# Kernel optimization log

Measured on AMD Instinct MI355X. Metric: run time of the kernel, lower is better.

Reference implementation:

```python
import jax, jax.numpy as jnp
import numpy as np

N_NODES = 100000
N_EDGES = 1600000
D_IN = 128
D_HID = 128
D_OUT = 64


def setup_inputs() -> dict:
    key = jax.random.key(0)
    ks = jax.random.split(key, 8)
    x = jax.random.normal(ks[0], (N_NODES, D_IN), dtype=jnp.float32)
    edge_index = jax.random.randint(ks[1], (2, N_EDGES), 0, N_NODES, dtype=jnp.int64)
    s1 = 1.0 / np.sqrt(D_IN)
    s2 = 1.0 / np.sqrt(D_HID)
    W1_l = jax.random.normal(ks[2], (D_IN, D_HID), dtype=jnp.float32) * s1
    W1_r = jax.random.normal(ks[3], (D_IN, D_HID), dtype=jnp.float32) * s1
    b1 = jnp.zeros((D_HID,), dtype=jnp.float32)
    W2_l = jax.random.normal(ks[4], (D_HID, D_OUT), dtype=jnp.float32) * s2
    W2_r = jax.random.normal(ks[5], (D_HID, D_OUT), dtype=jnp.float32) * s2
    b2 = jnp.zeros((D_OUT,), dtype=jnp.float32)
    return {"x": x, "edge_index": edge_index, "W1_l": W1_l, "b1": b1,
            "W1_r": W1_r, "W2_l": W2_l, "b2": b2, "W2_r": W2_r}


def _sage_conv(x, src, dst, Wl, bl, Wr, num_nodes):
    # PyG SAGEConv (aggr='mean', root_weight=True):
    #   out = lin_l(mean_{j in N(i)} x_j) + lin_r(x_i)
    agg = jax.ops.segment_sum(x[src], dst, num_segments=num_nodes)        # [N, d]
    deg = jax.ops.segment_sum(jnp.ones((src.shape[0],), dtype=x.dtype), dst,
                              num_segments=num_nodes)                      # [N]
    mean = agg / jnp.maximum(deg, 1.0)[:, None]
    return mean @ Wl + bl + x @ Wr


def reference(x, edge_index, W1_l, b1, W1_r, W2_l, b2, W2_r):
    src, dst = edge_index[0], edge_index[1]
    n = x.shape[0]
    h = jax.nn.relu(_sage_conv(x, src, dst, W1_l, b1, W1_r, n))
    # dropout is identity in eval mode
    out = _sage_conv(h, src, dst, W2_l, b2, W2_r, n)
    return jax.nn.log_softmax(out, axis=1)
```

## Files before the change

kernel.cpp:

```cpp
#include <hip/hip_runtime.h>
#include <math.h>

#define NN 100000
#define NE 1600000
#define SBN 512
#define NSB ((NN + SBN - 1) / SBN)
#define SBCAP 10240
#define EPB 8192
#define NBA ((NE + EPB - 1) / EPB)

typedef __attribute__((ext_vector_type(8))) short bf16x8;
typedef __attribute__((ext_vector_type(8))) unsigned short ush8;
typedef __attribute__((ext_vector_type(4))) float f32x4;

static __device__ __forceinline__ float b2f(unsigned short u) {
    return __uint_as_float(((unsigned int)u) << 16);
}
static __device__ __forceinline__ unsigned short f2bf(float f) {
    unsigned int u = __float_as_uint(f);
    u += 0x7fffu + ((u >> 16) & 1u);
    return (unsigned short)(u >> 16);
}

__global__ __launch_bounds__(256)
void k_cvt_x(const float* __restrict__ in, unsigned short* __restrict__ outb, long total8) {
    long i = (long)blockIdx.x * 256 + threadIdx.x;
    long stride = (long)gridDim.x * 256;
    for (; i < total8; i += stride) {
        const float4* p = (const float4*)(in + i * 8);
        float4 a = p[0], b = p[1];
        ush8 r;
        r[0] = f2bf(a.x); r[1] = f2bf(a.y); r[2] = f2bf(a.z); r[3] = f2bf(a.w);
        r[4] = f2bf(b.x); r[5] = f2bf(b.y); r[6] = f2bf(b.z); r[7] = f2bf(b.w);
        *(ush8*)(outb + i * 8) = r;
    }
}

__global__ __launch_bounds__(256)
void k_cvt_w(const float* __restrict__ W, unsigned short* __restrict__ Wt, int N) {
    int id = blockIdx.x * 256 + threadIdx.x;
    if (id < N * 128) {
        int n = id >> 7, k = id & 127;
        Wt[id] = f2bf(W[k * N + n]);
    }
}

__global__ __launch_bounds__(1024)
void k_binA(const int* __restrict__ src, const int* __restrict__ dst,
            int* __restrict__ gcnt, int* __restrict__ pairs) {
    __shared__ int lsort[EPB];
    __shared__ int lhist[256];
    __shared__ int lofs[256];
    __shared__ int lpos[NSB];
    __shared__ int gbase[NSB];
    const int tid = threadIdx.x;
    const int base = blockIdx.x * EPB;
    const int cnt = min(EPB, NE - base);

    int v[8], bn[8];
    #pragma unroll
    for (int k = 0; k < 8; ++k) {
        int i = k * 1024 + tid;
        if (i < cnt) {
            int d = dst[base + i], s = src[base + i];
            v[k] = (s << 9) | (d & 511);
            bn[k] = d >> 9;
        } else bn[k] = -1;
    }
    if (tid < 256) lhist[tid] = 0;
    __syncthreads();
    #pragma unroll
    for (int k = 0; k < 8; ++k) if (bn[k] >= 0) atomicAdd(&lhist[bn[k]], 1);
    __syncthreads();
    if (tid < 256) lofs[tid] = lhist[tid];
    __syncthreads();
    for (int d = 1; d < 256; d <<= 1) {
        int u = (tid < 256 && tid >= d) ? lofs[tid - d] : 0;
        __syncthreads();
        if (tid < 256) lofs[tid] += u;
        __syncthreads();
    }
    if (tid < 256) lofs[tid] -= lhist[tid];
    __syncthreads();
    if (tid < NSB) {
        lpos[tid] = lofs[tid];
        gbase[tid] = atomicAdd(&gcnt[tid], lhist[tid]);
    }
    __syncthreads();
    #pragma unroll
    for (int k = 0; k < 8; ++k) if (bn[k] >= 0) {
        int slot = atomicAdd(&lpos[bn[k]], 1);
        lsort[slot] = v[k];
    }
    __syncthreads();
    for (int i = tid; i < cnt; i += 1024) {
        int lo = 0, hi = NSB - 1;
        while (lo < hi) { int mid = (lo + hi + 1) >> 1; if (lofs[mid] <= i) lo = mid; else hi = mid - 1; }
        int off = gbase[lo] + (i - lofs[lo]);
        if (off < SBCAP)
            __builtin_nontemporal_store(lsort[i], &pairs[(size_t)lo * SBCAP + off]);
    }
}

__global__ __launch_bounds__(1024)
void k_sortB(const int* __restrict__ gcnt, int* __restrict__ pairs,
             int* __restrict__ offs, int* __restrict__ deg) {
    __shared__ int lstage[SBCAP];
    __shared__ int lhist[SBN], lscan[SBN], lpos[SBN];
    const int sb = blockIdx.x, tid = threadIdx.x;
    const int cnt = min(gcnt[sb], SBCAP);
    int* __restrict__ region = pairs + (size_t)sb * SBCAP;

    for (int i = tid; i < cnt; i += 1024) lstage[i] = region[i];
    if (tid < SBN) lhist[tid] = 0;
    __syncthreads();
    for (int i = tid; i < cnt; i += 1024) atomicAdd(&lhist[lstage[i] & 511], 1);
    __syncthreads();
    if (tid < SBN) lscan[tid] = lhist[tid];
    __syncthreads();
    for (int d = 1; d < SBN; d <<= 1) {
        int u = (tid < SBN && tid >= d) ? lscan[tid - d] : 0;
        __syncthreads();
        if (tid < SBN) lscan[tid] += u;
        __syncthreads();
    }
    if (tid < SBN) {
        int ex = lscan[tid] - lhist[tid];
        lpos[tid] = ex;
        int node = sb * SBN + tid;
        if (node < NN) { offs[node] = sb * SBCAP + ex; deg[node] = lhist[tid]; }
    }
    __syncthreads();
    for (int i = tid; i < cnt; i += 1024) {
        int val = lstage[i];
        int slot = atomicAdd(&lpos[val & 511], 1);
        region[slot] = val >> 9;
    }
}

__global__ __launch_bounds__(256)
void k_aggregate_bf(const unsigned short* __restrict__ feat, const int* __restrict__ csr,
                    const int* __restrict__ offs, const int* __restrict__ deg,
                    unsigned short* __restrict__ outmean) {
    const int wid = threadIdx.x >> 6, lane = threadIdx.x & 63;
    const int q = lane >> 4, l4 = lane & 15;
    const int node = blockIdx.x * 4 + wid;
    if (node >= NN) return;
    int off = __builtin_amdgcn_readfirstlane(offs[node]);
    int dg  = __builtin_amdgcn_readfirstlane(deg[node]);
    const ush8* __restrict__ f8 = (const ush8*)feat;
    float acc[8];
    #pragma unroll
    for (int i = 0; i < 8; ++i) acc[i] = 0.f;
    int j = 0;
    for (; j + 8 <= dg; j += 8) {
        int e0 = csr[off + j + q];
        int e1 = csr[off + j + 4 + q];
        ush8 v0 = f8[(size_t)e0 * 16 + l4];
        ush8 v1 = f8[(size_t)e1 * 16 + l4];
        #pragma unroll
        for (int i = 0; i < 8; ++i) acc[i] += b2f(v0[i]) + b2f(v1[i]);
    }
    for (; j + 4 <= dg; j += 4) {
        int e0 = csr[off + j + q];
        ush8 v0 = f8[(size_t)e0 * 16 + l4];
        #pragma unroll
        for (int i = 0; i < 8; ++i) acc[i] += b2f(v0[i]);
    }
    int rem = dg - j;
    if (q < rem) {
        int e0 = csr[off + j + q];
        ush8 v0 = f8[(size_t)e0 * 16 + l4];
        #pragma unroll
        for (int i = 0; i < 8; ++i) acc[i] += b2f(v0[i]);
    }
    #pragma unroll
    for (int i = 0; i < 8; ++i) {
        acc[i] += __shfl_xor(acc[i], 16);
        acc[i] += __shfl_xor(acc[i], 32);
    }
    if (q == 0) {
        float inv = 1.0f / (float)(dg > 0 ? dg : 1);
        ush8 r;
        #pragma unroll
        for (int i = 0; i < 8; ++i) r[i] = f2bf(acc[i] * inv);
        ((ush8*)outmean)[(size_t)node * 16 + l4] = r;
    }
}

template <int BN, bool RELU, bool OUTBF, bool LSM>
__global__ __launch_bounds__(256)
void k_gemm_mfma(const unsigned short* __restrict__ Am, const unsigned short* __restrict__ Ax,
                 const unsigned short* __restrict__ Wtl, const unsigned short* __restrict__ Wtr,
                 const float* __restrict__ bias, void* __restrict__ outp) {
    constexpr int BM = 128;
    constexpr int WAVES_N = BN / 64;
    constexpr int WAVES_M = 4 / WAVES_N;
    constexpr int MR = BM / (WAVES_M * 16);
    constexpr int NR = 4;
    __shared__ __align__(16) short As[BM * 40];
    __shared__ __align__(16) short Ws[BN * 40];

    const int tid = threadIdx.x;
    const int wave = tid >> 6, lane = tid & 63;
    const int l15 = lane & 15, kg = lane >> 4;
    const int wc = wave % WAVES_N, wr = wave / WAVES_N;
    const int rowbase = wr * MR * 16;
    const int colbase = wc * 64;
    const int row0 = blockIdx.x * BM;

    f32x4 acc[MR][NR];
    #pragma unroll
    for (int mr = 0; mr < MR; ++mr)
        #pragma unroll
        for (int nr = 0; nr < NR; ++nr) acc[mr][nr] = (f32x4){0.f, 0.f, 0.f, 0.f};

    for (int s = 0; s < 2; ++s) {
        const unsigned short* __restrict__ A  = s ? Ax : Am;
        const unsigned short* __restrict__ Wt = s ? Wtr : Wtl;
        for (int kc = 0; kc < 128; kc += 32) {
            __syncthreads();
            #pragma unroll
            for (int i = 0; i < (BM * 4) / 256; ++i) {
                int c = tid + 256 * i; int r = c >> 2, g = c & 3;
                ush8 v = {0, 0, 0, 0, 0, 0, 0, 0};
                int grow = row0 + r;
                if (grow < NN) v = *(const ush8*)&A[(size_t)grow * 128 + kc + g * 8];
                *(ush8*)&As[r * 40 + g * 8] = v;
            }
            #pragma unroll
            for (int i = 0; i < (BN * 4) / 256; ++i) {
                int c = tid + 256 * i; int n = c >> 2, g = c & 3;
                *(ush8*)&Ws[n * 40 + g * 8] = *(const ush8*)&Wt[n * 128 + kc + g * 8];
            }
            __syncthreads();
            bf16x8 af[MR], bfr[NR];
            #pragma unroll
            for (int mr = 0; mr < MR; ++mr)
                af[mr] = *(const bf16x8*)&As[(rowbase + mr * 16 + l15) * 40 + kg * 8];
            #pragma unroll
            for (int nr = 0; nr < NR; ++nr)
                bfr[nr] = *(const bf16x8*)&Ws[(colbase + nr * 16 + l15) * 40 + kg * 8];
            #pragma unroll
            for (int mr = 0; mr < MR; ++mr)
                #pragma unroll
                for (int nr = 0; nr < NR; ++nr)
                    acc[mr][nr] = __builtin_amdgcn_mfma_f32_16x16x32_bf16(
                        af[mr], bfr[nr], acc[mr][nr], 0, 0, 0);
        }
    }
    const int r4 = kg * 4;
    if (LSM) {
        #pragma unroll
        for (int mr = 0; mr < MR; ++mr) {
            #pragma unroll
            for (int j = 0; j < 4; ++j) {
                int row = row0 + rowbase + mr * 16 + r4 + j;
                float v[NR];
                float m = -1e30f;
                #pragma unroll
                for (int nr = 0; nr < NR; ++nr) {
                    v[nr] = acc[mr][nr][j] + bias[nr * 16 + l15];
                    m = fmaxf(m, v[nr]);
                }
                #pragma unroll
                for (int d = 8; d >= 1; d >>= 1) m = fmaxf(m, __shfl_xor(m, d));
                float ssum = 0.f;
                #pragma unroll
                for (int nr = 0; nr < NR; ++nr) ssum += __expf(v[nr] - m);
                #pragma unroll
                for (int d = 8; d >= 1; d >>= 1) ssum += __shfl_xor(ssum, d);
                float lse = m + logf(ssum);
                if (row < NN) {
                    #pragma unroll
                    for (int nr = 0; nr < NR; ++nr)
                        ((float*)outp)[(size_t)row * 64 + nr * 16 + l15] = v[nr] - lse;
                }
            }
        }
    } else {
        #pragma unroll
        for (int mr = 0; mr < MR; ++mr) {
            #pragma unroll
            for (int nr = 0; nr < NR; ++nr) {
                int col = colbase + nr * 16 + l15;
                float bv = bias[col];
                #pragma unroll
                for (int j = 0; j < 4; ++j) {
                    int row = row0 + rowbase + mr * 16 + r4 + j;
                    if (row < NN) {
                        float v = acc[mr][nr][j] + bv;
                        if (RELU) v = fmaxf(v, 0.f);
                        if (OUTBF) ((unsigned short*)outp)[(size_t)row * BN + col] = f2bf(v);
                        else       ((float*)outp)[(size_t)row * BN + col] = v;
                    }
                }
            }
        }
    }
}

extern "C" void kernel_launch(void* const* d_in, const int* in_sizes, int n_in,
                              void* d_out, int out_size, void* d_ws, size_t ws_size,
                              hipStream_t stream) {
    const float* x   = (const float*)d_in[0];
    const int* edges = (const int*)d_in[1];
    const float* W1l = (const float*)d_in[2];
    const float* b1  = (const float*)d_in[3];
    const float* W1r = (const float*)d_in[4];
    const float* W2l = (const float*)d_in[5];
    const float* b2  = (const float*)d_in[6];
    const float* W2r = (const float*)d_in[7];
    float* out = (float*)d_out;

    const int* src = edges;
    const int* dst = edges + NE;

    char* ws = (char*)d_ws;
    size_t o = 0;
    auto alloc = [&](size_t bytes) -> void* {
        void* p = ws + o;
        o = (o + bytes + 255) & ~(size_t)255;
        return p;
    };
    int* gcnt  = (int*)alloc((size_t)NSB * 4);
    int* pairs = (int*)alloc((size_t)NSB * SBCAP * 4);
    int* offs  = (int*)alloc((size_t)NN * 4);
    int* deg   = (int*)alloc((size_t)NN * 4);
    unsigned short* xb    = (unsigned short*)alloc((size_t)NN * 128 * 2);
    unsigned short* meanb = (unsigned short*)alloc((size_t)NN * 128 * 2);
    unsigned short* hb    = (unsigned short*)alloc((size_t)NN * 128 * 2);
    unsigned short* Wt1l  = (unsigned short*)alloc(128 * 128 * 2);
    unsigned short* Wt1r  = (unsigned short*)alloc(128 * 128 * 2);
    unsigned short* Wt2l  = (unsigned short*)alloc(64 * 128 * 2);
    unsigned short* Wt2r  = (unsigned short*)alloc(64 * 128 * 2);

    hipMemsetAsync(gcnt, 0, (size_t)NSB * 4, stream);

    k_cvt_x<<<2048, 256, 0, stream>>>(x, xb, (long)NN * 128 / 8);
    k_cvt_w<<<(128 * 128 + 255) / 256, 256, 0, stream>>>(W1l, Wt1l, 128);
    k_cvt_w<<<(128 * 128 + 255) / 256, 256, 0, stream>>>(W1r, Wt1r, 128);
    k_cvt_w<<<(64 * 128 + 255) / 256, 256, 0, stream>>>(W2l, Wt2l, 64);
    k_cvt_w<<<(64 * 128 + 255) / 256, 256, 0, stream>>>(W2r, Wt2r, 64);

    k_binA<<<NBA, 1024, 0, stream>>>(src, dst, gcnt, pairs);
    k_sortB<<<NSB, 1024, 0, stream>>>(gcnt, pairs, offs, deg);

    const int GEMM_GRID = (NN + 127) / 128;
    k_aggregate_bf<<<(NN + 3) / 4, 256, 0, stream>>>(xb, pairs, offs, deg, meanb);
    k_gemm_mfma<128, true, true, false><<<GEMM_GRID, 256, 0, stream>>>(meanb, xb, Wt1l, Wt1r, b1, hb);
    k_aggregate_bf<<<(NN + 3) / 4, 256, 0, stream>>>(hb, pairs, offs, deg, meanb);
    k_gemm_mfma<64, false, false, true><<<GEMM_GRID, 256, 0, stream>>>(meanb, hb, Wt2l, Wt2r, b2, out);
}
```

Baseline: 226.1 us.

## Transform before aggregating in layer 2 and fuse log-softmax into aggregation

Layer 2 now multiplies h by the concatenated [W2_l | W2_r] first, giving 64-wide projected features, and then aggregates only the 64-wide W2_l projection over neighbours. The mean, root term, bias and log-softmax are fused into a single aggregation kernel. This halves the bytes gathered per edge in the second aggregation and drops one GEMM input pass. The cost is an extra bf16 rounding of the projected values before they are averaged.

```diff
diff --git a/kernel.cpp b/kernel.cpp
--- a/kernel.cpp
+++ b/kernel.cpp
@@ -42,6 +42,17 @@
     if (id < N * 128) {
         int n = id >> 7, k = id & 127;
         Wt[id] = f2bf(W[k * N + n]);
+    }
+}
+
+__global__ __launch_bounds__(256)
+void k_cvt_wcat(const float* __restrict__ W2l, const float* __restrict__ W2r,
+                unsigned short* __restrict__ Wt) {
+    int id = blockIdx.x * 256 + threadIdx.x;
+    if (id < 128 * 128) {
+        int n = id >> 7, k = id & 127;
+        float v = (n < 64) ? W2l[k * 64 + n] : W2r[k * 64 + (n - 64)];
+        Wt[id] = f2bf(v);
     }
 }
 
@@ -188,7 +199,7 @@
     }
 }
 
-template <int BN, bool RELU, bool OUTBF, bool LSM>
+template <int BN, bool RELU, bool OUTBF>
 __global__ __launch_bounds__(256)
 void k_gemm_mfma(const unsigned short* __restrict__ Am, const unsigned short* __restrict__ Ax,
                  const unsigned short* __restrict__ Wtl, const unsigned short* __restrict__ Wtr,
@@ -250,53 +261,163 @@
         }
     }
     const int r4 = kg * 4;
-    if (LSM) {
-        #pragma unroll
-        for (int mr = 0; mr < MR; ++mr) {
+    #pragma unroll
+    for (int mr = 0; mr < MR; ++mr) {
+        #pragma unroll
+        for (int nr = 0; nr < NR; ++nr) {
+            int col = colbase + nr * 16 + l15;
+            float bv = bias[col];
             #pragma unroll
             for (int j = 0; j < 4; ++j) {
                 int row = row0 + rowbase + mr * 16 + r4 + j;
-                float v[NR];
-                float m = -1e30f;
-                #pragma unroll
-                for (int nr = 0; nr < NR; ++nr) {
-                    v[nr] = acc[mr][nr][j] + bias[nr * 16 + l15];
-                    m = fmaxf(m, v[nr]);
-                }
-                #pragma unroll
-                for (int d = 8; d >= 1; d >>= 1) m = fmaxf(m, __shfl_xor(m, d));
-                float ssum = 0.f;
-                #pragma unroll
-                for (int nr = 0; nr < NR; ++nr) ssum += __expf(v[nr] - m);
-                #pragma unroll
-                for (int d = 8; d >= 1; d >>= 1) ssum += __shfl_xor(ssum, d);
-                float lse = m + logf(ssum);
                 if (row < NN) {
-                    #pragma unroll
-                    for (int nr = 0; nr < NR; ++nr)
-                        ((float*)outp)[(size_t)row * 64 + nr * 16 + l15] = v[nr] - lse;
+                    float v = acc[mr][nr][j] + bv;
+                    if (RELU) v = fmaxf(v, 0.f);
+                    if (OUTBF) ((unsigned short*)outp)[(size_t)row * BN + col] = f2bf(v);
+                    else       ((float*)outp)[(size_t)row * BN + col] = v;
                 }
             }
         }
-    } else {
-        #pragma unroll
-        for (int mr = 0; mr < MR; ++mr) {
-            #pragma unroll
-            for (int nr = 0; nr < NR; ++nr) {
-                int col = colbase + nr * 16 + l15;
-                float bv = bias[col];
-                #pragma unroll
-                for (int j = 0; j < 4; ++j) {
-                    int row = row0 + rowbase + mr * 16 + r4 + j;
-                    if (row < NN) {
-                        float v = acc[mr][nr][j] + bv;
-                        if (RELU) v = fmaxf(v, 0.f);
-                        if (OUTBF) ((unsigned short*)outp)[(size_t)row * BN + col] = f2bf(v);
-                        else       ((float*)outp)[(size_t)row * BN + col] = v;
-                    }
+    }
+}
+
+__global__ __launch_bounds__(256)
+void k_gemm_cat(const unsigned short* __restrict__ A, const unsigned short* __restrict__ Wt,
+                const float* __restrict__ b2,
+                unsigned short* __restrict__ g, unsigned short* __restrict__ z) {
+    constexpr int BM = 128, BN = 128, MR = 4, NR = 4;
+    __shared__ __align__(16) short As[BM * 40];
+    __shared__ __align__(16) short Ws[BN * 40];
+
+    const int tid = threadIdx.x;
+    const int wave = tid >> 6, lane = tid & 63;
+    const int l15 = lane & 15, kg = lane >> 4;
+    const int wc = wave % 2, wr = wave / 2;
+    const int rowbase = wr * MR * 16;
+    const int colbase = wc * 64;
+    const int row0 = blockIdx.x * BM;
+
+    f32x4 acc[MR][NR];
+    #pragma unroll
+    for (int mr = 0; mr < MR; ++mr)
+        #pragma unroll
+        for (int nr = 0; nr < NR; ++nr) acc[mr][nr] = (f32x4){0.f, 0.f, 0.f, 0.f};
+
+    for (int kc = 0; kc < 128; kc += 32) {
+        __syncthreads();
+        #pragma unroll
+        for (int i = 0; i < 2; ++i) {
+            int c = tid + 256 * i; int r = c >> 2, gg = c & 3;
+            ush8 v = {0, 0, 0, 0, 0, 0, 0, 0};
+            int grow = row0 + r;
+            if (grow < NN) v = *(const ush8*)&A[(size_t)grow * 128 + kc + gg * 8];
+            *(ush8*)&As[r * 40 + gg * 8] = v;
+        }
+        #pragma unroll
+        for (int i = 0; i < 2; ++i) {
+            int c = tid + 256 * i; int n = c >> 2, gg = c & 3;
+            *(ush8*)&Ws[n * 40 + gg * 8] = *(const ush8*)&Wt[n * 128 + kc + gg * 8];
+        }
+        __syncthreads();
+        bf16x8 af[MR], bfr[NR];
+        #pragma unroll
+        for (int mr = 0; mr < MR; ++mr)
+            af[mr] = *(const bf16x8*)&As[(rowbase + mr * 16 + l15) * 40 + kg * 8];
+        #pragma unroll
+        for (int nr = 0; nr < NR; ++nr)
+            bfr[nr] = *(const bf16x8*)&Ws[(colbase + nr * 16 + l15) * 40 + kg * 8];
+        #pragma unroll
+        for (int mr = 0; mr < MR; ++mr)
+            #pragma unroll
+            for (int nr = 0; nr < NR; ++nr)
+                acc[mr][nr] = __builtin_amdgcn_mfma_f32_16x16x32_bf16(
+                    af[mr], bfr[nr], acc[mr][nr], 0, 0, 0);
+    }
+    const int r4 = kg * 4;
+    #pragma unroll
+    for (int mr = 0; mr < MR; ++mr) {
+        #pragma unroll
+        for (int nr = 0; nr < NR; ++nr) {
+            int col = colbase + nr * 16 + l15;
+            float bv = (col >= 64) ? b2[col - 64] : 0.f;
+            #pragma unroll
+            for (int j = 0; j < 4; ++j) {
+                int row = row0 + rowbase + mr * 16 + r4 + j;
+                if (row < NN) {
+                    float v = acc[mr][nr][j] + bv;
+                    unsigned short bv16 = f2bf(v);
+                    if (col < 64) g[(size_t)row * 64 + col] = bv16;
+                    else          z[(size_t)row * 64 + (col - 64)] = bv16;
                 }
             }
         }
+    }
+}
+
+__global__ __launch_bounds__(256)
+void k_agg_lsm(const unsigned short* __restrict__ gbuf, const unsigned short* __restrict__ zbuf,
+               const int* __restrict__ csr, const int* __restrict__ offs,
+               const int* __restrict__ deg, float* __restrict__ out) {
+    const int wid = threadIdx.x >> 6, lane = threadIdx.x & 63;
+    const int g8 = lane >> 3, l8 = lane & 7;
+    const int node = blockIdx.x * 4 + wid;
+    if (node >= NN) return;
+    int off = __builtin_amdgcn_readfirstlane(offs[node]);
+    int dg  = __builtin_amdgcn_readfirstlane(deg[node]);
+    const ush8* __restrict__ f8 = (const ush8*)gbuf;
+    float acc[8];
+    #pragma unroll
+    for (int i = 0; i < 8; ++i) acc[i] = 0.f;
+    int j = 0;
+    for (; j + 16 <= dg; j += 16) {
+        int e0 = csr[off + j + g8];
+        int e1 = csr[off + j + 8 + g8];
+        ush8 v0 = f8[(size_t)e0 * 8 + l8];
+        ush8 v1 = f8[(size_t)e1 * 8 + l8];
+        #pragma unroll
+        for (int i = 0; i < 8; ++i) acc[i] += b2f(v0[i]) + b2f(v1[i]);
+    }
+    for (; j + 8 <= dg; j += 8) {
+        int e0 = csr[off + j + g8];
+        ush8 v0 = f8[(size_t)e0 * 8 + l8];
+        #pragma unroll
+        for (int i = 0; i < 8; ++i) acc[i] += b2f(v0[i]);
+    }
+    int rem = dg - j;
+    if (g8 < rem) {
+        int e0 = csr[off + j + g8];
+        ush8 v0 = f8[(size_t)e0 * 8 + l8];
+        #pragma unroll
+        for (int i = 0; i < 8; ++i) acc[i] += b2f(v0[i]);
+    }
+    #pragma unroll
+    for (int i = 0; i < 8; ++i) {
+        acc[i] += __shfl_xor(acc[i], 8);
+        acc[i] += __shfl_xor(acc[i], 16);
+        acc[i] += __shfl_xor(acc[i], 32);
+    }
+    float inv = 1.0f / (float)(dg > 0 ? dg : 1);
+    ush8 zv = ((const ush8*)zbuf)[(size_t)node * 8 + l8];
+    float v[8];
+    float m = -1e30f;
+    #pragma unroll
+    for (int i = 0; i < 8; ++i) {
+        v[i] = acc[i] * inv + b2f(zv[i]);
+        m = fmaxf(m, v[i]);
+    }
+    #pragma unroll
+    for (int d = 4; d >= 1; d >>= 1) m = fmaxf(m, __shfl_xor(m, d));
+    float ss = 0.f;
+    #pragma unroll
+    for (int i = 0; i < 8; ++i) ss += __expf(v[i] - m);
+    #pragma unroll
+    for (int d = 4; d >= 1; d >>= 1) ss += __shfl_xor(ss, d);
+    float lse = m + logf(ss);
+    if (g8 == 0) {
+        float4 o0 = make_float4(v[0] - lse, v[1] - lse, v[2] - lse, v[3] - lse);
+        float4 o1 = make_float4(v[4] - lse, v[5] - lse, v[6] - lse, v[7] - lse);
+        *(float4*)&out[(size_t)node * 64 + l8 * 8]     = o0;
+        *(float4*)&out[(size_t)node * 64 + l8 * 8 + 4] = o1;
     }
 }
 
@@ -330,25 +451,25 @@
     unsigned short* xb    = (unsigned short*)alloc((size_t)NN * 128 * 2);
     unsigned short* meanb = (unsigned short*)alloc((size_t)NN * 128 * 2);
     unsigned short* hb    = (unsigned short*)alloc((size_t)NN * 128 * 2);
+    unsigned short* gbuf  = (unsigned short*)alloc((size_t)NN * 64 * 2);
+    unsigned short* zbuf  = (unsigned short*)alloc((size_t)NN * 64 * 2);
     unsigned short* Wt1l  = (unsigned short*)alloc(128 * 128 * 2);
     unsigned short* Wt1r  = (unsigned short*)alloc(128 * 128 * 2);
-    unsigned short* Wt2l  = (unsigned short*)alloc(64 * 128 * 2);
-    unsigned short* Wt2r  = (unsigned short*)alloc(64 * 128 * 2);
+    unsigned short* Wtcat = (unsigned short*)alloc(128 * 128 * 2);
 
     hipMemsetAsync(gcnt, 0, (size_t)NSB * 4, stream);
 
     k_cvt_x<<<2048, 256, 0, stream>>>(x, xb, (long)NN * 128 / 8);
     k_cvt_w<<<(128 * 128 + 255) / 256, 256, 0, stream>>>(W1l, Wt1l, 128);
     k_cvt_w<<<(128 * 128 + 255) / 256, 256, 0, stream>>>(W1r, Wt1r, 128);
-    k_cvt_w<<<(64 * 128 + 255) / 256, 256, 0, stream>>>(W2l, Wt2l, 64);
-    k_cvt_w<<<(64 * 128 + 255) / 256, 256, 0, stream>>>(W2r, Wt2r, 64);
+    k_cvt_wcat<<<(128 * 128 + 255) / 256, 256, 0, stream>>>(W2l, W2r, Wtcat);
 
     k_binA<<<NBA, 1024, 0, stream>>>(src, dst, gcnt, pairs);
     k_sortB<<<NSB, 1024, 0, stream>>>(gcnt, pairs, offs, deg);
 
     const int GEMM_GRID = (NN + 127) / 128;
     k_aggregate_bf<<<(NN + 3) / 4, 256, 0, stream>>>(xb, pairs, offs, deg, meanb);
-    k_gemm_mfma<128, true, true, false><<<GEMM_GRID, 256, 0, stream>>>(meanb, xb, Wt1l, Wt1r, b1, hb);
-    k_aggregate_bf<<<(NN + 3) / 4, 256, 0, stream>>>(hb, pairs, offs, deg, meanb);
-    k_gemm_mfma<64, false, false, true><<<GEMM_GRID, 256, 0, stream>>>(meanb, hb, Wt2l, Wt2r, b2, out);
-}
+    k_gemm_mfma<128, true, true><<<GEMM_GRID, 256, 0, stream>>>(meanb, xb, Wt1l, Wt1r, b1, hb);
+    k_gemm_cat<<<GEMM_GRID, 256, 0, stream>>>(hb, Wtcat, b2, gbuf, zbuf);
+    k_agg_lsm<<<(NN + 3) / 4, 256, 0, stream>>>(gbuf, zbuf, pairs, offs, deg, out);
+}
```

Result: no change. 224.0 us (-0.9%).
